# Optimization experiments

Measured on AMD Instinct MI355X. Metric: run time of the kernel, lower is better.

The kernel has to match this reference:

```python
import jax, jax.numpy as jnp
import numpy as np
from math import ceil

N, C_IN, HV, WV = 4, 3, 256, 256
C, K, NUM_LAYERS = 16, 3, 10
HK, WK = 45, 45
PROX_SCALE, KSCALE, KBSCALE, EPS = 10.0, 100.0, 0.01, 1e-8


def conv2_same(x, w):
    # torch F.conv2d (cross-correlation) with 'same' padding
    return jax.lax.conv_general_dilated(x, w, (1, 1), 'SAME',
                                        dimension_numbers=('NCHW', 'OIHW', 'NCHW'))


def pad_to(x, size):
    h, w = x.shape[-2], x.shape[-1]
    pads = [(0, 0)] * (x.ndim - 2) + [(0, size[0] - h), (0, size[1] - w)]
    return jnp.pad(x, pads)


def soft_threshold(x, b):
    return jnp.sign(x) * jax.nn.relu(jnp.abs(x) - b)


def circ_shift(x, s):
    return jnp.roll(x, (-s[0], -s[1]), axis=(-2, -1))


def csq(c):
    return (c * jnp.conj(c)).real


def forward(blurred_image, w0, ws, biases, kernel_biases, kernel_proxes, zetas, eta):
    Nb, C_in, Hv, Wv = blurred_image.shape
    Hs, Ws = Hv + HK - 1, Wv + WK - 1
    Hb, Wb = Hs + HK - 1, Ws + WK - 1
    fft_size = (int(ceil(Hb / 64.0) * 64), int(ceil(Wb / 64.0) * 64))
    rfft = lambda x: jnp.fft.rfft2(x, s=fft_size, axes=(-2, -1))
    irfft = lambda X: jnp.fft.irfft2(X, s=fft_size, axes=(-2, -1))

    # first-layer filter: zero-mean per (out,in) filter, then spatial reflect
    w_mean = w0.reshape(C, C_in, -1).mean(axis=-1)
    w0c = w0 - w_mean[:, :, None, None]
    w0_unreflected = jnp.transpose(w0c, (1, 0, 2, 3))   # (C_in, C, K, K)
    w0r = w0c[:, :, ::-1, ::-1]

    # analysis: cascade of convs, each feature stack padded to fft_size
    wy_list = []
    fy = blurred_image
    for layer in range(NUM_LAYERS):
        w = w0r if layer == 0 else ws[layer - 1]
        fy = conv2_same(fy, w)
        fy_p = pad_to(jnp.pad(fy, ((0, 0), (0, 0), (HK - 1, HK - 1), (WK - 1, WK - 1))), fft_size)
        wy_list.append(fy_p)

    delta = jnp.zeros((Nb, HK, WK), dtype=blurred_image.dtype).at[:, HK // 2, WK // 2].set(1.0)
    b0 = biases[0][None, :, None, None]
    z = soft_threshold(circ_shift(wy_list[-1], (HK // 2, WK // 2)), b0)
    Fz = rfft(z)
    k = delta
    Fg = None
    for layer in range(NUM_LAYERS):
        fy_p = wy_list.pop()
        Ffy = rfft(fy_p)                       # (N, C, H, Wf) complex
        Fk = rfft(k)[:, None]                  # (N, 1, H, Wf)
        zeta = PROX_SCALE * zetas[layer][None, :, None, None]
        num = zeta * (jnp.conj(Fk) * Ffy) + Fz
        den = zeta * csq(Fk) + 1.0
        Fg = num / (den + EPS)
        b = biases[layer + 1][None, :, None, None]
        z = soft_threshold(irfft(Fg), b)
        Fz = rfft(z)
        zk = kernel_proxes[layer]
        num_k = zk * jnp.sum(jnp.conj(Fz) * Ffy, axis=1) + Fk[:, 0]
        den_k = zk * jnp.sum(csq(Fz), axis=1) + 1.0
        k = irfft(num_k / (den_k + EPS))
        k_flat = k.reshape(Nb, -1)
        k_max = jax.scipy.special.logsumexp(k_flat * KSCALE, axis=-1) / KSCALE
        bk = KBSCALE * kernel_biases[layer]
        k = jax.nn.relu(k[:, :HK, :WK] - bk * k_max[:, None, None])
        k_sum = jnp.sum(k, axis=(1, 2), keepdims=True)
        k = (k + EPS * delta) / (k_sum + EPS)

    # final closed-form image solve in frequency domain (3-channel Cramer's rule)
    Fy = rfft(jnp.pad(blurred_image, ((0, 0), (0, 0), (HK - 1, HK - 1), (WK - 1, WK - 1))))
    Fk = rfft(k)                                # (N, H, Wf)
    Fw0 = rfft(circ_shift(pad_to(w0_unreflected, fft_size), (K // 2, K // 2)))  # (C_in, C, H, Wf)
    b_final = biases[NUM_LAYERS + 1][None, :, None, None]
    Fg = rfft(soft_threshold(irfft(Fg), b_final))

    eta_s = PROX_SCALE * eta[None, :, None, None]      # (1, C, 1, 1)
    Fwr, Fwg, Fwb = Fw0[0:1], Fw0[1:2], Fw0[2:3]       # (1, C, H, Wf)
    Fyr, Fyg, Fyb = Fy[:, 0], Fy[:, 1], Fy[:, 2]
    Fk_sq = csq(Fk)
    Crr = Fk_sq + jnp.sum(eta_s * csq(Fwr), axis=1)
    Cgg = Fk_sq + jnp.sum(eta_s * csq(Fwg), axis=1)
    Cbb = Fk_sq + jnp.sum(eta_s * csq(Fwb), axis=1)
    Crg = jnp.sum(eta_s * jnp.conj(Fwr) * Fwg, axis=1)
    Crb = jnp.sum(eta_s * jnp.conj(Fwr) * Fwb, axis=1)
    Cgb = jnp.sum(eta_s * jnp.conj(Fwg) * Fwb, axis=1)
    Fk_conj = jnp.conj(Fk)
    Br = Fk_conj * Fyr + jnp.sum(eta_s * jnp.conj(Fwr) * Fg, axis=1)
    Bg = Fk_conj * Fyg + jnp.sum(eta_s * jnp.conj(Fwg) * Fg, axis=1)
    Bb = Fk_conj * Fyb + jnp.sum(eta_s * jnp.conj(Fwb) * Fg, axis=1)
    Crg_sq, Crb_sq, Cgb_sq = csq(Crg), csq(Crb), csq(Cgb)
    Irr = Cgg * Cbb - Cgb_sq
    Igg = Crr * Cbb - Crb_sq
    Ibb = Crr * Cgg - Crg_sq
    Irg = jnp.conj(Cgb) * Crb - Cbb * Crg
    Irb = Crg * Cgb - Cgg * Crb
    Igb = jnp.conj(Crg) * Crb - Crr * Cgb
    den = (Crr * (Cgg * Cbb - Cgb_sq) - Cgg * Crb_sq - Cbb * Crg_sq
           + 2 * (Crg * Cgb * jnp.conj(Crb)).real) + EPS
    Fxr = Irr * Br + Irg * Bg + Irb * Bb
    Fxg = jnp.conj(Irg) * Br + Igg * Bg + Igb * Bb
    Fxb = jnp.conj(Irb) * Br + jnp.conj(Igb) * Bg + Ibb * Bb
    Fx = jnp.stack([Fxr, Fxg, Fxb], axis=1) / den[:, None]

    image = irfft(Fx)[:, :, HK // 2:HK // 2 + Hv, WK // 2:WK // 2 + Wv]
    return image, k


def setup_inputs() -> dict:
    key = jax.random.key(0)
    ks = jax.random.split(key, 4)

    def xavier(k, shape, fan_in, fan_out):
        std = (2.0 / (fan_in + fan_out)) ** 0.5
        return std * jax.random.normal(k, shape, dtype=jnp.float32)

    return {
        'blurred_image': jax.random.normal(ks[0], (N, C_IN, HV, WV), dtype=jnp.float32),
        'w0': xavier(ks[1], (C, C_IN, K, K), C_IN * K * K, C * K * K),
        'ws': xavier(ks[2], (NUM_LAYERS - 1, C, C, 3, 3), C * 9, C * 9),
        'biases': jnp.full((NUM_LAYERS + 2, C), 0.02, dtype=jnp.float32),
        'kernel_biases': jnp.zeros((NUM_LAYERS,), dtype=jnp.float32),
        'kernel_proxes': jnp.ones((NUM_LAYERS,), dtype=jnp.float32),
        'zetas': jnp.ones((NUM_LAYERS, C), dtype=jnp.float32),
        'eta': jnp.ones((C,), dtype=jnp.float32),
    }


def reference(blurred_image, w0, ws, biases, kernel_biases, kernel_proxes, zetas, eta):
    return forward(blurred_image, w0, ws, biases, kernel_biases, kernel_proxes, zetas, eta)
```

## Files before the change

kernel.cpp:

```cpp
#include <hip/hip_runtime.h>
#include <math.h>

#define FH 384
#define KF 193
#define KS 384
#define SPW 147456

typedef __attribute__((ext_vector_type(8))) short short8;
typedef __attribute__((ext_vector_type(4))) float f32x4;
typedef unsigned int u32;
typedef unsigned short u16;

static __device__ __forceinline__ float softt(float v, float b) {
    return copysignf(fmaxf(fabsf(v) - b, 0.f), v);
}
static __device__ __forceinline__ u16 bf16_rn(float v) {
    u32 u = __float_as_uint(v);
    u32 r = (u + 0x7FFFu + ((u >> 16) & 1u)) >> 16;
    return (u16)r;
}
static __device__ __forceinline__ float bf16_to_f(u16 h) {
    return __uint_as_float(((u32)h) << 16);
}
static __device__ __forceinline__ float2 ldc(const uint2* __restrict__ S, size_t i) {
    uint2 u = S[i];
    float2 r;
    r.x = __uint_as_float((u.x & 0xffffu) << 16) + __uint_as_float((u.y & 0xffffu) << 16);
    r.y = __uint_as_float(u.x & 0xffff0000u) + __uint_as_float(u.y & 0xffff0000u);
    return r;
}
static __device__ __forceinline__ uint2 packc(float re, float im) {
    u16 hr = bf16_rn(re), hi = bf16_rn(im);
    u16 lr = bf16_rn(re - bf16_to_f(hr)), li = bf16_rn(im - bf16_to_f(hi));
    uint2 o; o.x = (u32)hr | ((u32)hi << 16); o.y = (u32)lr | ((u32)li << 16);
    return o;
}

__global__ void init_ef_k(float2* Ef) {
    int idx = blockIdx.x * 256 + threadIdx.x;
    if (idx >= FH * FH) return;
    int h = idx / FH, j = idx % FH;
    int m = (h * j) % FH;
    float th = (float)(6.283185307179586 / FH) * (float)m;
    float2 v; v.x = cosf(th); v.y = -sinf(th);
    Ef[idx] = v;
}

__global__ void init_estack192(u16* __restrict__ H, u16* __restrict__ L, int inv)
{
    int idx = blockIdx.x * 256 + threadIdx.x;
    if (idx >= KS * KS) return;
    int gm = idx / KS, kp = idx % KS;
    int m = gm >> 1, comp = gm & 1;
    int t = kp >> 1, ri = kp & 1;
    int mm = (m * t) % 192;
    float th = (float)(6.283185307179586 / 192.0) * (float)mm;
    float c = cosf(th), s = sinf(th);
    float er, ei;
    if (inv) { er = c * (1.f/384.f); ei = s * (1.f/384.f); }
    else     { er = c;               ei = -s; }
    float v;
    if (comp == 0) v = (ri == 0) ? er : -ei;
    else           v = (ri == 0) ? ei :  er;
    u16 h = bf16_rn(v);
    H[idx] = h;
    L[idx] = bf16_rn(v - bf16_to_f(h));
}

// ... 54 lines not shown
    const u16*   iL  = inL0 ? inL0 + iofs : nullptr;
    u16* oH = outH0 + (size_t)blockIdx.z * 16*65536;
    u16* oL = outL0 + (size_t)blockIdx.z * 16*65536;
    __shared__ float tile[18][19];
    __shared__ float wl[16*16*9];
    int x0 = blockIdx.x * 16, y0 = blockIdx.y * 16;
    int t = threadIdx.x;
    int tx = t & 15, ty = t >> 4;
    int nw = 16 * Cin * 9;
    for (int i = t; i < nw; i += 256) {
        int d = i % 9;
        wl[i] = flip ? w[i + 8 - 2*d] : w[i];
    }
    float acc[16];
#pragma unroll
    for (int co = 0; co < 16; ++co) acc[co] = 0.f;
    for (int ci = 0; ci < Cin; ++ci) {
        __syncthreads();
        for (int i = t; i < 18*18; i += 256) {
            int yy = i / 18, xx = i % 18;
            int gy = y0 - 1 + yy, gx = x0 - 1 + xx;
            float v = 0.f;
            if (gy >= 0 && gy < 256 && gx >= 0 && gx < 256) {
                size_t ii = ((size_t)ci*256 + gy)*256 + gx;
                v = inF ? inF[ii] : (bf16_to_f(iH[ii]) + bf16_to_f(iL[ii]));
            }
            tile[yy][xx] = v;
        }
        __syncthreads();
        float v[9];
#pragma unroll
        for (int dy = 0; dy < 3; dy++)
#pragma unroll
            for (int dx = 0; dx < 3; dx++) v[dy*3+dx] = tile[ty+dy][tx+dx];
#pragma unroll
        for (int co = 0; co < 16; co++) {
            const float* wp = &wl[(co*Cin+ci)*9];
            acc[co] += v[0]*wp[0]+v[1]*wp[1]+v[2]*wp[2]
                     + v[3]*wp[3]+v[4]*wp[4]+v[5]*wp[5]
                     + v[6]*wp[6]+v[7]*wp[7]+v[8]*wp[8];
        }
    }
#pragma unroll
    for (int co = 0; co < 16; co++) {
        size_t o = ((size_t)co*256 + (y0+ty))*256 + (x0+tx);
        u16 h = bf16_rn(acc[co]);
        oH[o] = h;
        oL[o] = bf16_rn(acc[co] - bf16_to_f(h));
    }
}

__global__ void zinit_kernel(const u16* __restrict__ fy9H, const u16* __restrict__ fy9L,
                             const float* __restrict__ b0, float* __restrict__ z, int total)
{
    int idx = blockIdx.x*256 + threadIdx.x;
    if (idx >= total) return;
    int x = idx % FH; int r = idx / FH; int y = r % FH; int plane = r / FH;
    int c = plane & 15;
    int Y = y + 22; if (Y >= FH) Y -= FH;
    int X = x + 22; if (X >= FH) X -= FH;
    int yy = Y - 44, xx = X - 44;
    float v = 0.f;
    if (yy >= 0 && yy < 256 && xx >= 0 && xx < 256) {
        size_t ii = ((size_t)plane*256 + yy)*256 + xx;
        v = bf16_to_f(fy9H[ii]) + bf16_to_f(fy9L[ii]);
    }
    z[idx] = softt(v, b0[c]);
}

static __device__ __forceinline__ void r2c192_epilogue(
    f32x4 accA[2][4], f32x4 accB[2][4],
    int col0, int njN, int y0, int wave, int lm, int lq,
    uint2* __restrict__ outp, int B, int plane)
{
#pragma unroll
    for (int mi = 0; mi < 2; ++mi) {
#pragma unroll
        for (int nj = 0; nj < 4; ++nj) {
            if (nj >= njN) continue;
            int n = col0 + nj*16 + lm;
            int j = n >> 1;
            float pA[4], pB[4];
#pragma unroll
            for (int rr = 0; rr < 4; ++rr) {
                pA[rr] = __shfl_xor(accA[mi][nj][rr], 1);
                pB[rr] = __shfl_xor(accB[mi][nj][rr], 1);
            }
            if (((lm & 1) == 0) && j <= 96) {
                float th = (float)(6.283185307179586 / 384.0) * (float)j;
                float sv, cv;
                __sincosf(th, &sv, &cv);
                float wr = cv, wi = -sv;
                int ybase = y0 + wave*32 + mi*16 + lq*4;
#pragma unroll
                for (int rr = 0; rr < 4; ++rr) {
                    float ar = accA[mi][nj][rr], ai = pA[rr];
                    float br = accB[mi][nj][rr], bi = pB[rr];
                    float tr = wr*br - wi*bi;
                    float ti = wr*bi + wi*br;
                    size_t rowb = ((size_t)(ybase+rr)*B + plane)*KF;
                    outp[rowb + j] = packc(ar + tr, ai + ti);
                    if (j < 96) outp[rowb + 192 - j] = packc(ar - tr, -(ai - ti));
                }
            }
        }
    }
}

__global__ __launch_bounds__(256) void r2c192_f(
    const float* __restrict__ inp, int inH, int inW, int offY, int offX,
    const float* __restrict__ thr,
    const u16* __restrict__ TH, const u16* __restrict__ TL,
    uint2* __restrict__ outp, int B)
{
    __shared__ u16 AhS[2][8*64*8];
    __shared__ u16 AlS[2][8*64*8];
    int col0 = blockIdx.x * 64;
    int y0   = blockIdx.y * 128;
    int plane = blockIdx.z;
    int njN = (col0 >= 192) ? 1 : 4;
    int tid = threadIdx.x;
    int wave = tid >> 6, lane = tid & 63;
    int lm = lane & 15, lq = lane >> 4;
    f32x4 accA[2][4], accB[2][4];
#pragma unroll
    for (int mi = 0; mi < 2; ++mi)
#pragma unroll
        for (int nj = 0; nj < 4; ++nj) {
            accA[mi][nj] = (f32x4){0.f,0.f,0.f,0.f};
            accB[mi][nj] = (f32x4){0.f,0.f,0.f,0.f};
        }
    float bthr = thr ? thr[plane & 15] : 0.f;
    const float* inpP = inp + (size_t)plane*inH*inW;
    int mhi = (offX + inW) >> 1;
    for (int kt = 0; kt < mhi; kt += 32) {
#pragma unroll
        for (int s = 0; s < 4; ++s) {
            int slot = tid + s*256;
            int r = slot >> 3, kq = slot & 7;
            int yy = y0 + r - offY;
            int xx0 = 2*(kt + kq*4) - offX;
            float v[8];
#pragma unroll
            for (int d = 0; d < 8; ++d) {
                int xx = xx0 + d;
                float t = 0.f;
                if (yy >= 0 && yy < inH && xx >= 0 && xx < inW)
                    t = inpP[(size_t)yy*inW + xx];
                if (thr) t = softt(t, bthr);
                v[d] = t;
            }
            u16 h[8], l[8];
#pragma unroll
            for (int d = 0; d < 8; ++d) {
                h[d] = bf16_rn(v[d]);
                l[d] = bf16_rn(v[d] - bf16_to_f(h[d]));
            }
            int base = ((r >> 4)*64 + (r & 15) + 16*(kq >> 1))*8 + (kq & 1)*4;
            uint2 w;
            w.x = (u32)h[0] | ((u32)h[2] << 16); w.y = (u32)h[4] | ((u32)h[6] << 16);
            *(uint2*)&AhS[0][base] = w;
            w.x = (u32)h[1] | ((u32)h[3] << 16); w.y = (u32)h[5] | ((u32)h[7] << 16);
            *(uint2*)&AhS[1][base] = w;
            w.x = (u32)l[0] | ((u32)l[2] << 16); w.y = (u32)l[4] | ((u32)l[6] << 16);
            *(uint2*)&AlS[0][base] = w;
            w.x = (u32)l[1] | ((u32)l[3] << 16); w.y = (u32)l[5] | ((u32)l[7] << 16);
            *(uint2*)&AlS[1][base] = w;
        }
        __syncthreads();
        short8 A0h[2], A0l[2], A1h[2], A1l[2];
#pragma unroll
// ... 2 lines not shown
            A0h[mi] = *(const short8*)&AhS[0][fo];
            A0l[mi] = *(const short8*)&AlS[0][fo];
            A1h[mi] = *(const short8*)&AhS[1][fo];
            A1l[mi] = *(const short8*)&AlS[1][fo];
        }
#pragma unroll
        for (int nj = 0; nj < 4; ++nj) {
            if (nj >= njN) continue;
            size_t toff = (size_t)(col0 + nj*16 + lm)*192 + kt + lq*8;
            short8 Bh = *(const short8*)(TH + toff);
            short8 Bl = *(const short8*)(TL + toff);
#pragma unroll
            for (int mi = 0; mi < 2; ++mi) {
                accA[mi][nj] = __builtin_amdgcn_mfma_f32_16x16x32_bf16(A0h[mi], Bh, accA[mi][nj], 0, 0, 0);
                accA[mi][nj] = __builtin_amdgcn_mfma_f32_16x16x32_bf16(A0h[mi], Bl, accA[mi][nj], 0, 0, 0);
                accA[mi][nj] = __builtin_amdgcn_mfma_f32_16x16x32_bf16(A0l[mi], Bh, accA[mi][nj], 0, 0, 0);
                accB[mi][nj] = __builtin_amdgcn_mfma_f32_16x16x32_bf16(A1h[mi], Bh, accB[mi][nj], 0, 0, 0);
                accB[mi][nj] = __builtin_amdgcn_mfma_f32_16x16x32_bf16(A1h[mi], Bl, accB[mi][nj], 0, 0, 0);
                accB[mi][nj] = __builtin_amdgcn_mfma_f32_16x16x32_bf16(A1l[mi], Bh, accB[mi][nj], 0, 0, 0);
            }
        }
        __syncthreads();
    }
    r2c192_epilogue(accA, accB, col0, njN, y0, wave, lm, lq, outp, B, plane);
}

__global__ __launch_bounds__(256) void r2c192_s(
    const u16* __restrict__ Hs, const u16* __restrict__ Ls,
    int inH, int inW, int offY, int offX,
    const u16* __restrict__ TH, const u16* __restrict__ TL,
    uint2* __restrict__ outp, int B)
{
    __shared__ u16 AhS[2][8*64*8];
    __shared__ u16 AlS[2][8*64*8];
    int col0 = blockIdx.x * 64;
    int y0   = blockIdx.y * 128;
    int plane = blockIdx.z;
    int njN = (col0 >= 192) ? 1 : 4;
    int tid = threadIdx.x;
    int wave = tid >> 6, lane = tid & 63;
    int lm = lane & 15, lq = lane >> 4;
    f32x4 accA[2][4], accB[2][4];
#pragma unroll
    for (int mi = 0; mi < 2; ++mi)
#pragma unroll
        for (int nj = 0; nj < 4; ++nj) {
            accA[mi][nj] = (f32x4){0.f,0.f,0.f,0.f};
            accB[mi][nj] = (f32x4){0.f,0.f,0.f,0.f};
        }
    const u16* hP = Hs + (size_t)plane*inH*inW;
    const u16* lP = Ls + (size_t)plane*inH*inW;
    int mhi = (offX + inW) >> 1;
    for (int kt = 0; kt < mhi; kt += 32) {
#pragma unroll
        for (int s = 0; s < 4; ++s) {
            int slot = tid + s*256;
            int r = slot >> 3, kq = slot & 7;
            int yy = y0 + r - offY;
            int xx0 = 2*(kt + kq*4) - offX;
            uint2 hlo, hhi, llo, lhi;
            hlo.x=hlo.y=hhi.x=hhi.y=0u; llo.x=llo.y=lhi.x=lhi.y=0u;
            bool yok = (yy >= 0 && yy < inH);
            if (yok && xx0 >= 0 && xx0 + 4 <= inW) {
                size_t o = (size_t)yy*inW + xx0;
                hlo = *(const uint2*)(hP + o);
                llo = *(const uint2*)(lP + o);
            }
            if (yok && xx0 + 4 >= 0 && xx0 + 8 <= inW) {
                size_t o = (size_t)yy*inW + xx0 + 4;
                hhi = *(const uint2*)(hP + o);
                lhi = *(const uint2*)(lP + o);
            }
            int base = ((r >> 4)*64 + (r & 15) + 16*(kq >> 1))*8 + (kq & 1)*4;
            uint2 w;
            w.x = (hlo.x & 0xffffu) | (hlo.y << 16);
            w.y = (hhi.x & 0xffffu) | (hhi.y << 16);
            *(uint2*)&AhS[0][base] = w;
            w.x = (hlo.x >> 16) | (hlo.y & 0xffff0000u);
            w.y = (hhi.x >> 16) | (hhi.y & 0xffff0000u);
            *(uint2*)&AhS[1][base] = w;
            w.x = (llo.x & 0xffffu) | (llo.y << 16);
            w.y = (lhi.x & 0xffffu) | (lhi.y << 16);
            *(uint2*)&AlS[0][base] = w;
            w.x = (llo.x >> 16) | (llo.y & 0xffff0000u);
            w.y = (lhi.x >> 16) | (lhi.y & 0xffff0000u);
            *(uint2*)&AlS[1][base] = w;
        }
        __syncthreads();
        short8 A0h[2], A0l[2], A1h[2], A1l[2];
#pragma unroll
        for (int mi = 0; mi < 2; ++mi) {
            int fo = ((wave*2 + mi)*64 + lane)*8;
            A0h[mi] = *(const short8*)&AhS[0][fo];
            A0l[mi] = *(const short8*)&AlS[0][fo];
            A1h[mi] = *(const short8*)&AhS[1][fo];
            A1l[mi] = *(const short8*)&AlS[1][fo];
        }
#pragma unroll
        for (int nj = 0; nj < 4; ++nj) {
            if (nj >= njN) continue;
            size_t toff = (size_t)(col0 + nj*16 + lm)*192 + kt + lq*8;
            short8 Bh = *(const short8*)(TH + toff);
            short8 Bl = *(const short8*)(TL + toff);
#pragma unroll
            for (int mi = 0; mi < 2; ++mi) {
                accA[mi][nj] = __builtin_amdgcn_mfma_f32_16x16x32_bf16(A0h[mi], Bh, accA[mi][nj], 0, 0, 0);
                accA[mi][nj] = __builtin_amdgcn_mfma_f32_16x16x32_bf16(A0h[mi], Bl, accA[mi][nj], 0, 0, 0);
                accA[mi][nj] = __builtin_amdgcn_mfma_f32_16x16x32_bf16(A0l[mi], Bh, accA[mi][nj], 0, 0, 0);
                accB[mi][nj] = __builtin_amdgcn_mfma_f32_16x16x32_bf16(A1h[mi], Bh, accB[mi][nj], 0, 0, 0);
                accB[mi][nj] = __builtin_amdgcn_mfma_f32_16x16x32_bf16(A1h[mi], Bl, accB[mi][nj], 0, 0, 0);
                accB[mi][nj] = __builtin_amdgcn_mfma_f32_16x16x32_bf16(A1l[mi], Bh, accB[mi][nj], 0, 0, 0);
            }
        }
        __syncthreads();
    }
    r2c192_epilogue(accA, accB, col0, njN, y0, wave, lm, lq, outp, B, plane);
}

__global__ void gpm_kernel(uint2* __restrict__ S, int rows)
{
    int idx = blockIdx.x*256 + threadIdx.x;
    if (idx >= rows * 97) return;
    int j = idx % 97;
    size_t b = (size_t)(idx / 97) * KF;
    if (j == 96) {
        float2 f = ldc(S, b + 96);
        S[b + 96] = packc(2.f*f.x, -2.f*f.y);
    } else {
        float2 f1 = ldc(S, b + j);
        float2 f2 = ldc(S, b + 192 - j);
        float gpx = f1.x + f2.x, gpy = f1.y - f2.y;
        float hx  = f1.x - f2.x, hy  = f1.y + f2.y;
        float th = (float)(6.283185307179586 / 384.0) * (float)j;
        float sv, cv;
        __sincosf(th, &sv, &cv);
        float gmx = cv*hx - sv*hy;
        float gmy = cv*hy + sv*hx;
        S[b + j]       = packc(gpx, gpy);
        S[b + 192 - j] = packc(gmx, gmy);
    }
}

__global__ __launch_bounds__(256) void c2r192(
    const uint2* __restrict__ Ain,
    const u16* __restrict__ UH, const u16* __restrict__ UL,
    float* __restrict__ outp, const float* __restrict__ thr,
    u16* __restrict__ spH, u16* __restrict__ spL, int B)
{
    __shared__ u16 AhS[2][8*64*8];
    __shared__ u16 AlS[2][8*64*8];
    int col0 = blockIdx.x * 64;
    int y0   = blockIdx.y * 128;
    int plane = blockIdx.z;
    int tid = threadIdx.x;
    int wave = tid >> 6, lane = tid & 63;
    int lm = lane & 15, lq = lane >> 4;
    f32x4 accP[2][4], accQ[2][4];
#pragma unroll
    for (int mi = 0; mi < 2; ++mi)
#pragma unroll
// ... 58 lines not shown
                accQ[mi][nj] = __builtin_amdgcn_mfma_f32_16x16x32_bf16(A1h[mi], Bl, accQ[mi][nj], 0, 0, 0);
                accQ[mi][nj] = __builtin_amdgcn_mfma_f32_16x16x32_bf16(A1l[mi], Bh, accQ[mi][nj], 0, 0, 0);
            }
        }
        __syncthreads();
    }
    float bthr = thr ? thr[plane & 15] : 0.f;
#pragma unroll
    for (int mi = 0; mi < 2; ++mi) {
#pragma unroll
        for (int nj = 0; nj < 4; ++nj) {
            int m = col0 + nj*16 + lm;
#pragma unroll
            for (int rr = 0; rr < 4; ++rr) {
                int y = y0 + wave*32 + mi*16 + lq*4 + rr;
                float xe = accP[mi][nj][rr];
                float xo = accQ[mi][nj][rr];
                float2 o2; o2.x = xe; o2.y = xo;
                *(float2*)&outp[((size_t)plane*FH + y)*FH + 2*m] = o2;
                if (spH) {
                    float s0 = softt(xe, bthr), s1 = softt(xo, bthr);
                    u16 h0 = bf16_rn(s0), h1 = bf16_rn(s1);
                    u16 l0 = bf16_rn(s0 - bf16_to_f(h0)), l1 = bf16_rn(s1 - bf16_to_f(h1));
                    size_t d = (size_t)plane*SPW + (size_t)y*FH + 2*m;
                    *(u32*)&spH[d] = (u32)h0 | ((u32)h1 << 16);
                    *(u32*)&spL[d] = (u32)l0 | ((u32)l1 << 16);
                }
            }
        }
    }
}

__global__ __launch_bounds__(256) void zgemm_col_mfma2(
    const u16* __restrict__ EH, const u16* __restrict__ EL,
    const uint2* __restrict__ Bm, uint2* __restrict__ Cm, int N, float sgn)
{
    __shared__ u16 BhS[2][4*64*8];
    __shared__ u16 BlS[2][4*64*8];
    int col0 = blockIdx.x * 64;
    int row0 = blockIdx.y * 128;
    int tid = threadIdx.x;
    int wave = tid >> 6, lane = tid & 63;
    int lm = lane & 15, lq = lane >> 4;
    f32x4 accE[2][4], accO[2][4];
#pragma unroll
    for (int mi = 0; mi < 2; ++mi)
#pragma unroll
        for (int nj = 0; nj < 4; ++nj) {
            accE[mi][nj] = (f32x4){0.f,0.f,0.f,0.f};
            accO[mi][nj] = (f32x4){0.f,0.f,0.f,0.f};
        }
    int arow0 = row0 + wave*32 + lm;
    for (int kt = 0; kt < KS; kt += 32) {
        int tbase = kt >> 1;
#pragma unroll
        for (int s = 0; s < 4; ++s) {
            int slot = tid + s*256;
            int p    = slot >> 9;
            int inr  = slot & 511;
            int pair = inr >> 6;
            int n    = inr & 63;
            int gn   = col0 + n;
            int t0   = tbase + pair*2;
            uint2 u0, u1;
            u0.x = u0.y = u1.x = u1.y = 0u;
            if (gn < N) {
                u0 = Bm[(size_t)(2*t0 + p)*N + gn];
                u1 = Bm[(size_t)(2*t0 + 2 + p)*N + gn];
            }
            int ntile = n >> 4, n0 = n & 15;
            int lrow  = (pair >> 1)*16 + n0;
            int base  = (ntile*64 + lrow)*8 + (pair & 1)*4;
            uint2 hp, lp;
            hp.x = u0.x; hp.y = u1.x;
            lp.x = u0.y; lp.y = u1.y;
            *(uint2*)&BhS[p][base] = hp;
// ... 18 lines not shown
                accE[mi][nj] = __builtin_amdgcn_mfma_f32_16x16x32_bf16(Ah[mi], Bh0, accE[mi][nj], 0, 0, 0);
                accE[mi][nj] = __builtin_amdgcn_mfma_f32_16x16x32_bf16(Ah[mi], Bl0, accE[mi][nj], 0, 0, 0);
                accE[mi][nj] = __builtin_amdgcn_mfma_f32_16x16x32_bf16(Al[mi], Bh0, accE[mi][nj], 0, 0, 0);
                accO[mi][nj] = __builtin_amdgcn_mfma_f32_16x16x32_bf16(Ah[mi], Bh1, accO[mi][nj], 0, 0, 0);
                accO[mi][nj] = __builtin_amdgcn_mfma_f32_16x16x32_bf16(Ah[mi], Bl1, accO[mi][nj], 0, 0, 0);
                accO[mi][nj] = __builtin_amdgcn_mfma_f32_16x16x32_bf16(Al[mi], Bh1, accO[mi][nj], 0, 0, 0);
            }
        }
        __syncthreads();
    }
#pragma unroll
    for (int mi = 0; mi < 2; ++mi) {
#pragma unroll
        for (int nj = 0; nj < 4; ++nj) {
            int coln = col0 + nj*16 + lm;
            if (coln < N) {
                int r0 = row0 + wave*32 + mi*16 + lq*4;
                int h  = r0 >> 1;
#pragma unroll
                for (int pp = 0; pp < 2; ++pp) {
                    float e_re = accE[mi][nj][2*pp],   e_im = accE[mi][nj][2*pp+1];
                    float o_re = accO[mi][nj][2*pp],   o_im = accO[mi][nj][2*pp+1];
                    int hh = h + pp;
                    float th = (float)(6.283185307179586 / 384.0) * (float)hh;
                    float sv, cv;
                    __sincosf(th, &sv, &cv);
                    float twr = cv, twi = sgn * sv;
                    float tr = twr*o_re - twi*o_im;
                    float ti = twr*o_im + twi*o_re;
                    Cm[(size_t)hh*N + coln]         = packc(e_re + tr, e_im + ti);
                    Cm[(size_t)(hh + 192)*N + coln] = packc(e_re - tr, e_im - ti);
                }
            }
        }
    }
}

__global__ void fg_kernel(const uint2* __restrict__ Ffy, uint2* __restrict__ Fz,
                          const uint2* __restrict__ Fk, const float* __restrict__ zetas,
                          int L, int total)
{
    int idx = blockIdx.x*256 + threadIdx.x;
    if (idx >= total) return;
    int k = idx % KF; int r = idx / KF;
    int c = r & 15; int hi = r >> 4;
    float zeta = 10.f * zetas[L*16 + c];
    float2 fk = ldc(Fk, (size_t)hi*KF + k);
    float2 fy = ldc(Ffy, idx);
    float2 fz = ldc(Fz, idx);
    float nx = zeta*(fk.x*fy.x + fk.y*fy.y) + fz.x;
// ... 37 lines not shown
{
    int img = blockIdx.y;
    const float* kraw = kraw0 + (size_t)img*FH*FH;
    int b = blockIdx.x, t = threadIdx.x;
    float m = -1e30f, s = 0.f;
    for (int i = b*256 + t; i < FH*FH; i += 64*256) {
        float v = 100.f * kraw[i];
        lse_comb(m, s, v, 1.f);
    }
    __shared__ float sm[256], ss[256];
    sm[t] = m; ss[t] = s;
    __syncthreads();
    for (int st = 128; st > 0; st >>= 1) {
        if (t < st) {
            float mm = sm[t], sc = ss[t];
            lse_comb(mm, sc, sm[t+st], ss[t+st]);
            sm[t] = mm; ss[t] = sc;
        }
        __syncthreads();
    }
    if (t == 0) { float2 o; o.x = sm[0]; o.y = ss[0]; parts[img*64 + b] = o; }
}

__global__ void lse_final_kernel(const float2* __restrict__ parts, float* __restrict__ kmaxB)
{
    int img = blockIdx.x;
    int t = threadIdx.x;
    __shared__ float sm[64], ss[64];
    float2 p = parts[img*64 + t];
    sm[t] = p.x; ss[t] = p.y;
    __syncthreads();
    for (int st = 32; st > 0; st >>= 1) {
        if (t < st) {
            float mm = sm[t], sc = ss[t];
            lse_comb(mm, sc, sm[t+st], ss[t+st]);
            sm[t] = mm; ss[t] = sc;
        }
        __syncthreads();
    }
    if (t == 0) kmaxB[img] = (sm[0] + logf(ss[0])) * 0.01f;
}

__global__ void zero_kernel(float* __restrict__ p, int n)
{
    int i = blockIdx.x*256 + threadIdx.x;
    if (i < n) p[i] = 0.f;
}

__global__ void kdelta_kernel(float* __restrict__ kful, int G)
{
    int t = threadIdx.x;
    if (t < G) kful[(size_t)t*FH*FH + 22*FH + 22] = 1.f;
}

__global__ __launch_bounds__(256) void knew_kernel(const float* __restrict__ kraw0,
    const float* __restrict__ kmax, const float* __restrict__ kb, int L,
    float* __restrict__ kful0)
{
    int img = blockIdx.x;
    const float* kraw = kraw0 + (size_t)img*FH*FH;
    float*       kful = kful0 + (size_t)img*FH*FH;
    int t = threadIdx.x;
    float thr = 0.01f * kb[L] * kmax[img];
    float vs[8]; float loc = 0.f;
#pragma unroll
    for (int ii = 0; ii < 8; ++ii) {
        int i = t + ii*256;
        float v = 0.f;
        if (i < 45*45) {
            int y = i/45, x = i - y*45;
            v = fmaxf(kraw[y*FH + x] - thr, 0.f);
        }
        vs[ii] = v; loc += v;
    }
    __shared__ float sr[256];
    sr[t] = loc; __syncthreads();
    for (int st = 128; st > 0; st >>= 1) { if (t < st) sr[t] += sr[t+st]; __syncthreads(); }
    float den = sr[0] + 1e-8f;
#pragma unroll
    for (int ii = 0; ii < 8; ++ii) {
        int i = t + ii*256;
        if (i < 45*45) {
            int y = i/45, x = i - y*45;
            float v = vs[ii] + ((y == 22 && x == 22) ? 1e-8f : 0.f);
            kful[y*FH + x] = v / den;
        }
// ... 108 lines not shown
    int x = rem % 45; int y = rem / 45;
    outp[idx] = kful[(size_t)img*FH*FH + y*FH + x];
}

extern "C" void kernel_launch(void* const* d_in, const int* in_sizes, int n_in,
                              void* d_out, int out_size, void* d_ws, size_t ws_size,
                              hipStream_t stream)
{
    (void)in_sizes; (void)n_in; (void)out_size;
    const float* blurred = (const float*)d_in[0];
    const float* w0      = (const float*)d_in[1];
    const float* wsw     = (const float*)d_in[2];
    const float* biases  = (const float*)d_in[3];
    const float* kbias   = (const float*)d_in[4];
    const float* kprox   = (const float*)d_in[5];
    const float* zetas   = (const float*)d_in[6];
    const float* eta     = (const float*)d_in[7];
    float* outp = (float*)d_out;

    auto al = [](size_t b) { return (b + 255) & ~(size_t)255; };
    auto need = [&](int G) -> size_t {
        size_t s = 0;
        s += al((size_t)FH*FH*8);
        s += 4*al((size_t)KS*KS*2);
        s += 2*al((size_t)208*192*2);
        s += 2*al((size_t)192*224*2);
        s += al(432*4);
        s += 2*al((size_t)10*G*16*65536*2);
        s += al((size_t)G*16*FH*FH*4);
        s += 2*al((size_t)G*16*SPW*2);
        s += 3*al((size_t)G*16*FH*KF*8);
        s += 3*al((size_t)G*FH*KF*8);
        s += 2*al((size_t)G*FH*FH*4);
        s += 2*al((size_t)G*3*FH*KF*8);
        s += al((size_t)G*64*8) + al(256);
        return s;
    };
    int G = 4;
    while (G > 1 && need(G) > ws_size) G >>= 1;

    char* base = (char*)d_ws;
    size_t off = 0;
    auto alloc = [&](size_t bytes) -> void* {
        void* p = (void*)(base + off);
        off += (bytes + 255) & ~(size_t)255;
        return p;
    };
    float2* Ef   = (float2*)alloc((size_t)FH*FH*8);
    u16* EfH = (u16*)alloc((size_t)KS*KS*2);
    u16* EfL = (u16*)alloc((size_t)KS*KS*2);
    u16* EiH = (u16*)alloc((size_t)KS*KS*2);
    u16* EiL = (u16*)alloc((size_t)KS*KS*2);
    u16* T1H = (u16*)alloc((size_t)208*192*2);
    u16* T1L = (u16*)alloc((size_t)208*192*2);
    u16* U1H = (u16*)alloc((size_t)192*224*2);
    u16* U1L = (u16*)alloc((size_t)192*224*2);
    float*  w0cB = (float*)alloc(432*4);
    u16*    fyH  = (u16*)alloc((size_t)10*G*16*65536*2);
    u16*    fyL  = (u16*)alloc((size_t)10*G*16*65536*2);
    float*  zsp  = (float*)alloc((size_t)G*16*FH*FH*4);
    u16*    zspSH= (u16*)alloc((size_t)G*16*SPW*2);
    u16*    zspSL= (u16*)alloc((size_t)G*16*SPW*2);
    uint2*  mid  = (uint2*)alloc((size_t)G*16*FH*KF*8);
    uint2*  FzFg = (uint2*)alloc((size_t)G*16*FH*KF*8);
    uint2*  Ffy  = (uint2*)alloc((size_t)G*16*FH*KF*8);
    uint2*  Fk   = (uint2*)alloc((size_t)G*FH*KF*8);
    uint2*  kfA  = (uint2*)alloc((size_t)G*FH*KF*8);
    uint2*  kfB  = (uint2*)alloc((size_t)G*FH*KF*8);
    float*  kraw = (float*)alloc((size_t)G*FH*FH*4);
    float*  kful = (float*)alloc((size_t)G*FH*FH*4);
    uint2*  FyB  = (uint2*)alloc((size_t)G*3*FH*KF*8);
    uint2*  FxB  = (uint2*)alloc((size_t)G*3*FH*KF*8);
    float2* lseP = (float2*)alloc((size_t)G*64*8);
    float*  kmaxB= (float*)alloc(256);
    float2* Fw0B = (float2*)fyH;

    init_ef_k<<<(FH*FH+255)/256, 256, 0, stream>>>(Ef);
    init_estack192<<<(KS*KS+255)/256, 256, 0, stream>>>(EfH, EfL, 0);
    init_estack192<<<(KS*KS+255)/256, 256, 0, stream>>>(EiH, EiL, 1);
    init_t192<<<(208*192+255)/256, 256, 0, stream>>>(T1H, T1L);
    init_u192<<<(192*224+255)/256, 256, 0, stream>>>(U1H, U1L);
    w0c_kernel<<<1, 64, 0, stream>>>(w0, w0cB);

    auto zgf = [&](const uint2* Bm, uint2* Cm, int Ncols) {
        zgemm_col_mfma2<<<dim3((Ncols+63)/64, 3), 256, 0, stream>>>(
            EfH, EfL, Bm, Cm, Ncols, -1.f);
    };
    auto zgi = [&](const uint2* Bm, uint2* Cm, int Ncols) {
        zgemm_col_mfma2<<<dim3((Ncols+63)/64, 3), 256, 0, stream>>>(
            EiH, EiL, Bm, Cm, Ncols, 1.f);
    };
    auto r2c = [&](const float* inp, int inH, int inW, int oY, int oX,
                   const float* thr, uint2* o, int B) {
        r2c192_f<<<dim3(4, 3, B), 256, 0, stream>>>(
            inp, inH, inW, oY, oX, thr, T1H, T1L, o, B);
    };
    auto r2cs = [&](const u16* Hs, const u16* Ls, int inH, int inW, int oY, int oX,
                    uint2* o, int B) {
        r2c192_s<<<dim3(4, 3, B), 256, 0, stream>>>(
            Hs, Ls, inH, inW, oY, oX, T1H, T1L, o, B);
    };
    auto c2r = [&](uint2* Ain, float* o, int B,
                   const float* thr, u16* sH, u16* sL) {
        int rows = FH * B;
        gpm_kernel<<<(rows*97 + 255)/256, 256, 0, stream>>>(Ain, rows);
        c2r192<<<dim3(3, 3, B), 256, 0, stream>>>(
            Ain, U1H, U1L, o, thr, sH, sL, B);
    };

    const size_t CKL = (size_t)G*16*65536;

    for (int g0 = 0; g0 < 4; g0 += G) {
        const float* img = blurred + (size_t)g0*3*65536;

        conv3x3_kernel<<<dim3(16,16,G), 256, 0, stream>>>(
            img, nullptr, nullptr, w0cB, fyH, fyL, 3, 1, (size_t)3*65536);
        for (int l = 1; l < 10; ++l)
            conv3x3_kernel<<<dim3(16,16,G), 256, 0, stream>>>(
                nullptr, fyH + (size_t)(l-1)*CKL, fyL + (size_t)(l-1)*CKL,
                wsw + (size_t)(l-1)*2304,
                fyH + (size_t)l*CKL, fyL + (size_t)l*CKL, 16, 0, (size_t)16*65536);

        int totZ = G*16*FH*FH;
        zinit_kernel<<<(totZ+255)/256, 256, 0, stream>>>(
            fyH + 9*CKL, fyL + 9*CKL, biases, zsp, totZ);
        r2c(zsp, FH, FH, 0, 0, nullptr, mid, G*16);
        zgf(mid, FzFg, G*16*KF);

        zero_kernel<<<(G*FH*FH+255)/256, 256, 0, stream>>>(kful, G*FH*FH);
        kdelta_kernel<<<1, 64, 0, stream>>>(kful, G);

        int totS = G*16*FH*KF;
        int totK = G*FH*KF;
        for (int it = 0; it < 10; ++it) {
            int Lfy = 9 - it;
            r2cs(fyH + (size_t)Lfy*CKL, fyL + (size_t)Lfy*CKL, 256, 256, 44, 44, mid, G*16);
            zgf(mid, Ffy, G*16*KF);
            r2c(kful, FH, FH, 0, 0, nullptr, mid, G);
            zgf(mid, Fk, G*KF);
            fg_kernel<<<(totS+255)/256, 256, 0, stream>>>(Ffy, FzFg, Fk, zetas, it, totS);
            zgi(FzFg, mid, G*16*KF);
            c2r(mid, zsp, G*16, biases + (it+1)*16, zspSH, zspSL);
            r2cs(zspSH, zspSL, FH, FH, 0, 0, mid, G*16);
            zgf(mid, FzFg, G*16*KF);
            knum_kernel<<<(totK+255)/256, 256, 0, stream>>>(FzFg, Ffy, Fk, kprox, it, totK, kfA);
            zgi(kfA, kfB, G*KF);
            c2r(kfB, kraw, G, nullptr, nullptr, nullptr);
            lse_part_kernel<<<dim3(64,G), 256, 0, stream>>>(kraw, lseP);
            lse_final_kernel<<<G, 64, 0, stream>>>(lseP, kmaxB);
            knew_kernel<<<G, 256, 0, stream>>>(kraw, kmaxB, kbias, it, kful);
        }

        r2c(img, 256, 256, 44, 44, nullptr, mid, 3*G);
        zgf(mid, FyB, 3*G*KF);
        r2c(kful, FH, FH, 0, 0, nullptr, mid, G);
        zgf(mid, Fk, G*KF);
        r2c(zsp, FH, FH, 0, 0, biases + 11*16, mid, G*16);
        zgf(mid, FzFg, G*16*KF);
        fw0_kernel<<<(48*FH*KF+255)/256, 256, 0, stream>>>(w0cB, Ef, Fw0B);
        wiener_kernel<<<(totK+255)/256, 256, 0, stream>>>(Fk, FyB, Fw0B, FzFg, eta, G, totK, FxB);
        zgi(FxB, mid, 3*G*KF);
        c2r(mid, zsp, 3*G, nullptr, nullptr, nullptr);
        int totC = G*3*65536;
        crop_kernel<<<(totC+255)/256, 256, 0, stream>>>(zsp, outp + (size_t)g0*3*65536, totC);
        int totKC = G*2025;
        kcopy_kernel<<<(totKC+255)/256, 256, 0, stream>>>(kful, outp + 786432 + g0*2025, totKC);
    }
}
```

Measured before the change: 8.760 ms.

## De-interleave bf16 split storage, prune kernel FFT, table twiddles, fuse LSE final

Conv outputs, the z init buffer and the c2r sparse outputs are now stored with even and odd columns in separate half-rows. This lets r2c192_s load 8 contiguous bf16 values with 16-byte vector loads instead of gathering and repacking in registers. The kernel-estimate FFT only transforms the 45x45 support: one row block, and the column GEMM's K loop is cut to 64. Twiddle sincos calls are replaced by a precomputed table, and lse_final is folded into knew_kernel to save one launch per iteration. The risks are layout mismatches between producers and consumers, and scalar u16 stores in c2r in place of packed u32 stores.

```diff
diff --git a/kernel.cpp b/kernel.cpp
--- a/kernel.cpp
+++ b/kernel.cpp
@@ -44,6 +44,15 @@
     float th = (float)(6.283185307179586 / FH) * (float)m;
     float2 v; v.x = cosf(th); v.y = -sinf(th);
     Ef[idx] = v;
+}
+
+__global__ void init_tw(float2* twT) {
+    int i = blockIdx.x * 256 + threadIdx.x;
+    if (i < 193) {
+        float th = (float)(6.283185307179586 / 384.0) * (float)i;
+        float2 v; v.x = cosf(th); v.y = sinf(th);
+        twT[i] = v;
+    }
 }
 
 __global__ void init_estack192(u16* __restrict__ H, u16* __restrict__ L, int inv)
@@ -144,7 +153,9 @@
             int gy = y0 - 1 + yy, gx = x0 - 1 + xx;
             float v = 0.f;
             if (gy >= 0 && gy < 256 && gx >= 0 && gx < 256) {
-                size_t ii = ((size_t)ci*256 + gy)*256 + gx;
+                size_t ii;
+                if (inF) ii = ((size_t)ci*256 + gy)*256 + gx;
+                else     ii = ((size_t)ci*256 + gy)*256 + ((gx>>1) + (gx&1)*128);
                 v = inF ? inF[ii] : (bf16_to_f(iH[ii]) + bf16_to_f(iL[ii]));
             }
             tile[yy][xx] = v;
@@ -163,9 +174,11 @@
                      + v[6]*wp[6]+v[7]*wp[7]+v[8]*wp[8];
         }
     }
+    int xo = x0 + tx;
+    int xd = (xo >> 1) + (xo & 1)*128;
 #pragma unroll
     for (int co = 0; co < 16; co++) {
-        size_t o = ((size_t)co*256 + (y0+ty))*256 + (x0+tx);
+        size_t o = ((size_t)co*256 + (y0+ty))*256 + xd;
         u16 h = bf16_rn(acc[co]);
         oH[o] = h;
         oL[o] = bf16_rn(acc[co] - bf16_to_f(h));
@@ -173,7 +186,8 @@
 }
 
 __global__ void zinit_kernel(const u16* __restrict__ fy9H, const u16* __restrict__ fy9L,
-                             const float* __restrict__ b0, float* __restrict__ z, int total)
+                             const float* __restrict__ b0,
+                             u16* __restrict__ oH, u16* __restrict__ oL, int total)
 {
     int idx = blockIdx.x*256 + threadIdx.x;
     if (idx >= total) return;
@@ -184,15 +198,20 @@
     int yy = Y - 44, xx = X - 44;
     float v = 0.f;
     if (yy >= 0 && yy < 256 && xx >= 0 && xx < 256) {
-        size_t ii = ((size_t)plane*256 + yy)*256 + xx;
+        size_t ii = ((size_t)plane*256 + yy)*256 + ((xx>>1) + (xx&1)*128);
         v = bf16_to_f(fy9H[ii]) + bf16_to_f(fy9L[ii]);
     }
-    z[idx] = softt(v, b0[c]);
+    float s = softt(v, b0[c]);
+    u16 h = bf16_rn(s);
+    size_t d = (size_t)plane*SPW + (size_t)y*FH + ((x>>1) + (x&1)*192);
+    oH[d] = h;
+    oL[d] = bf16_rn(s - bf16_to_f(h));
 }
 
 static __device__ __forceinline__ void r2c192_epilogue(
     f32x4 accA[2][4], f32x4 accB[2][4],
     int col0, int njN, int y0, int wave, int lm, int lq,
+    const float2* __restrict__ twT,
     uint2* __restrict__ outp, int B, int plane)
 {
 #pragma unroll
@@ -209,10 +228,8 @@
                 pB[rr] = __shfl_xor(accB[mi][nj][rr], 1);
             }
             if (((lm & 1) == 0) && j <= 96) {
-                float th = (float)(6.283185307179586 / 384.0) * (float)j;
-                float sv, cv;
-                __sincosf(th, &sv, &cv);
-                float wr = cv, wi = -sv;
+                float2 tw = twT[j];
+                float wr = tw.x, wi = -tw.y;
                 int ybase = y0 + wave*32 + mi*16 + lq*4;
 #pragma unroll
                 for (int rr = 0; rr < 4; ++rr) {
@@ -230,9 +247,11 @@
 }
 
 __global__ __launch_bounds__(256) void r2c192_f(
-    const float* __restrict__ inp, int inH, int inW, int offY, int offX,
+    const float* __restrict__ inp, int inH, int inW, int inStride, size_t planeStride,
+    int offY, int offX,
     const float* __restrict__ thr,
     const u16* __restrict__ TH, const u16* __restrict__ TL,
+    const float2* __restrict__ twT,
     uint2* __restrict__ outp, int B)
 {
     __shared__ u16 AhS[2][8*64*8];
@@ -253,7 +272,7 @@
             accB[mi][nj] = (f32x4){0.f,0.f,0.f,0.f};
         }
     float bthr = thr ? thr[plane & 15] : 0.f;
-    const float* inpP = inp + (size_t)plane*inH*inW;
+    const float* inpP = inp + (size_t)plane*planeStride;
     int mhi = (offX + inW) >> 1;
     for (int kt = 0; kt < mhi; kt += 32) {
 #pragma unroll
@@ -268,7 +287,7 @@
                 int xx = xx0 + d;
                 float t = 0.f;
                 if (yy >= 0 && yy < inH && xx >= 0 && xx < inW)
-                    t = inpP[(size_t)yy*inW + xx];
+                    t = inpP[(size_t)yy*inStride + xx];
                 if (thr) t = softt(t, bthr);
                 v[d] = t;
             }
@@ -317,13 +336,14 @@
         }
         __syncthreads();
     }
-    r2c192_epilogue(accA, accB, col0, njN, y0, wave, lm, lq, outp, B, plane);
+    r2c192_epilogue(accA, accB, col0, njN, y0, wave, lm, lq, twT, outp, B, plane);
 }
 
 __global__ __launch_bounds__(256) void r2c192_s(
     const u16* __restrict__ Hs, const u16* __restrict__ Ls,
     int inH, int inW, int offY, int offX,
     const u16* __restrict__ TH, const u16* __restrict__ TL,
+    const float2* __restrict__ twT,
     uint2* __restrict__ outp, int B)
 {
     __shared__ u16 AhS[2][8*64*8];
@@ -345,41 +365,48 @@
         }
     const u16* hP = Hs + (size_t)plane*inH*inW;
     const u16* lP = Ls + (size_t)plane*inH*inW;
+    int W2  = inW >> 1;
+    int ox2 = offX >> 1;
+    bool al16 = ((ox2 & 7) == 0);
     int mhi = (offX + inW) >> 1;
     for (int kt = 0; kt < mhi; kt += 32) {
 #pragma unroll
         for (int s = 0; s < 4; ++s) {
             int slot = tid + s*256;
-            int r = slot >> 3, kq = slot & 7;
+            int p    = slot >> 9;
+            int inr  = slot & 511;
+            int r = inr >> 2, kq2 = inr & 3;
             int yy = y0 + r - offY;
-            int xx0 = 2*(kt + kq*4) - offX;
-            uint2 hlo, hhi, llo, lhi;
-            hlo.x=hlo.y=hhi.x=hhi.y=0u; llo.x=llo.y=lhi.x=lhi.y=0u;
-            bool yok = (yy >= 0 && yy < inH);
-            if (yok && xx0 >= 0 && xx0 + 4 <= inW) {
-                size_t o = (size_t)yy*inW + xx0;
-                hlo = *(const uint2*)(hP + o);
-                llo = *(const uint2*)(lP + o);
-            }
-            if (yok && xx0 + 4 >= 0 && xx0 + 8 <= inW) {
-                size_t o = (size_t)yy*inW + xx0 + 4;
-                hhi = *(const uint2*)(hP + o);
-                lhi = *(const uint2*)(lP + o);
-            }
-            int base = ((r >> 4)*64 + (r & 15) + 16*(kq >> 1))*8 + (kq & 1)*4;
-            uint2 w;
-            w.x = (hlo.x & 0xffffu) | (hlo.y << 16);
-            w.y = (hhi.x & 0xffffu) | (hhi.y << 16);
-            *(uint2*)&AhS[0][base] = w;
-            w.x = (hlo.x >> 16) | (hlo.y & 0xffff0000u);
-            w.y = (hhi.x >> 16) | (hhi.y & 0xffff0000u);
-            *(uint2*)&AhS[1][base] = w;
-            w.x = (llo.x & 0xffffu) | (llo.y << 16);
-            w.y = (lhi.x & 0xffffu) | (lhi.y << 16);
-            *(uint2*)&AlS[0][base] = w;
-            w.x = (llo.x >> 16) | (llo.y & 0xffff0000u);
-            w.y = (lhi.x >> 16) | (lhi.y & 0xffff0000u);
-            *(uint2*)&AlS[1][base] = w;
+            int m0 = kt + kq2*8;
+            int pos = m0 - ox2;
+            uint4 hq = {0u,0u,0u,0u}, lq4 = {0u,0u,0u,0u};
+            if (yy >= 0 && yy < inH) {
+                const u16* hr = hP + (size_t)yy*inW + (size_t)p*W2;
+                const u16* lr = lP + (size_t)yy*inW + (size_t)p*W2;
+                if (pos >= 0 && pos + 8 <= W2) {
+                    if (al16) {
+                        hq  = *(const uint4*)(hr + pos);
+                        lq4 = *(const uint4*)(lr + pos);
+                    } else {
+                        hq.x = *(const u32*)(hr+pos);   hq.y = *(const u32*)(hr+pos+2);
+                        hq.z = *(const u32*)(hr+pos+4); hq.w = *(const u32*)(hr+pos+6);
+                        lq4.x = *(const u32*)(lr+pos);   lq4.y = *(const u32*)(lr+pos+2);
+                        lq4.z = *(const u32*)(lr+pos+4); lq4.w = *(const u32*)(lr+pos+6);
+                    }
+                } else if (pos + 8 > 0 && pos < W2) {
+#pragma unroll
+                    for (int q = 0; q < 4; ++q) {
+                        int pp = pos + 2*q;
+                        if (pp >= 0 && pp + 2 <= W2) {
+                            ((u32*)&hq)[q]  = *(const u32*)(hr+pp);
+                            ((u32*)&lq4)[q] = *(const u32*)(lr+pp);
+                        }
+                    }
+                }
+            }
+            int base = ((r >> 4)*64 + (r & 15) + 16*kq2)*8;
+            *(uint4*)&AhS[p][base] = hq;
+            *(uint4*)&AlS[p][base] = lq4;
         }
         __syncthreads();
         short8 A0h[2], A0l[2], A1h[2], A1l[2];
@@ -409,10 +436,10 @@
         }
         __syncthreads();
     }
-    r2c192_epilogue(accA, accB, col0, njN, y0, wave, lm, lq, outp, B, plane);
-}
-
-__global__ void gpm_kernel(uint2* __restrict__ S, int rows)
+    r2c192_epilogue(accA, accB, col0, njN, y0, wave, lm, lq, twT, outp, B, plane);
+}
+
+__global__ void gpm_kernel(uint2* __restrict__ S, const float2* __restrict__ twT, int rows)
 {
     int idx = blockIdx.x*256 + threadIdx.x;
     if (idx >= rows * 97) return;
@@ -426,11 +453,9 @@
         float2 f2 = ldc(S, b + 192 - j);
         float gpx = f1.x + f2.x, gpy = f1.y - f2.y;
         float hx  = f1.x - f2.x, hy  = f1.y + f2.y;
-        float th = (float)(6.283185307179586 / 384.0) * (float)j;
-        float sv, cv;
-        __sincosf(th, &sv, &cv);
-        float gmx = cv*hx - sv*hy;
-        float gmy = cv*hy + sv*hx;
+        float2 tw = twT[j];
+        float gmx = tw.x*hx - tw.y*hy;
+        float gmy = tw.x*hy + tw.y*hx;
         S[b + j]       = packc(gpx, gpy);
         S[b + 192 - j] = packc(gmx, gmy);
     }
@@ -535,9 +560,9 @@
                     float s0 = softt(xe, bthr), s1 = softt(xo, bthr);
                     u16 h0 = bf16_rn(s0), h1 = bf16_rn(s1);
                     u16 l0 = bf16_rn(s0 - bf16_to_f(h0)), l1 = bf16_rn(s1 - bf16_to_f(h1));
-                    size_t d = (size_t)plane*SPW + (size_t)y*FH + 2*m;
-                    *(u32*)&spH[d] = (u32)h0 | ((u32)h1 << 16);
-                    *(u32*)&spL[d] = (u32)l0 | ((u32)l1 << 16);
+                    size_t d = (size_t)plane*SPW + (size_t)y*FH + m;
+                    spH[d]       = h0; spL[d]       = l0;
+                    spH[d + 192] = h1; spL[d + 192] = l1;
                 }
             }
         }
@@ -546,7 +571,8 @@
 
 __global__ __launch_bounds__(256) void zgemm_col_mfma2(
     const u16* __restrict__ EH, const u16* __restrict__ EL,
-    const uint2* __restrict__ Bm, uint2* __restrict__ Cm, int N, float sgn)
+    const uint2* __restrict__ Bm, uint2* __restrict__ Cm, int N, float sgn,
+    int ktHi, const float2* __restrict__ twT)
 {
     __shared__ u16 BhS[2][4*64*8];
     __shared__ u16 BlS[2][4*64*8];
@@ -564,7 +590,7 @@
             accO[mi][nj] = (f32x4){0.f,0.f,0.f,0.f};
         }
     int arow0 = row0 + wave*32 + lm;
-    for (int kt = 0; kt < KS; kt += 32) {
+    for (int kt = 0; kt < ktHi; kt += 32) {
         int tbase = kt >> 1;
 #pragma unroll
         for (int s = 0; s < 4; ++s) {
@@ -629,10 +655,8 @@
                     float e_re = accE[mi][nj][2*pp],   e_im = accE[mi][nj][2*pp+1];
                     float o_re = accO[mi][nj][2*pp],   o_im = accO[mi][nj][2*pp+1];
                     int hh = h + pp;
-                    float th = (float)(6.283185307179586 / 384.0) * (float)hh;
-                    float sv, cv;
-                    __sincosf(th, &sv, &cv);
-                    float twr = cv, twi = sgn * sv;
+                    float2 tw = twT[hh];
+                    float twr = tw.x, twi = sgn * tw.y;
                     float tr = twr*o_re - twi*o_im;
                     float ti = twr*o_im + twi*o_re;
                     Cm[(size_t)hh*N + coln]         = packc(e_re + tr, e_im + ti);
@@ -716,13 +740,28 @@
     if (t == 0) { float2 o; o.x = sm[0]; o.y = ss[0]; parts[img*64 + b] = o; }
 }
 
-__global__ void lse_final_kernel(const float2* __restrict__ parts, float* __restrict__ kmaxB)
+__global__ void zero_kernel(float* __restrict__ p, int n)
+{
+    int i = blockIdx.x*256 + threadIdx.x;
+    if (i < n) p[i] = 0.f;
+}
+
+__global__ void kdelta_kernel(float* __restrict__ kful, int G)
+{
+    int t = threadIdx.x;
+    if (t < G) kful[(size_t)t*FH*FH + 22*FH + 22] = 1.f;
+}
+
+__global__ __launch_bounds__(256) void knew_kernel(const float2* __restrict__ parts,
+    const float* __restrict__ kraw0, const float* __restrict__ kb, int L,
+    float* __restrict__ kful0)
 {
     int img = blockIdx.x;
+    const float* kraw = kraw0 + (size_t)img*FH*FH;
+    float*       kful = kful0 + (size_t)img*FH*FH;
     int t = threadIdx.x;
     __shared__ float sm[64], ss[64];
-    float2 p = parts[img*64 + t];
-    sm[t] = p.x; ss[t] = p.y;
+    if (t < 64) { float2 p = parts[img*64 + t]; sm[t] = p.x; ss[t] = p.y; }
     __syncthreads();
     for (int st = 32; st > 0; st >>= 1) {
         if (t < st) {
@@ -732,30 +771,8 @@
         }
         __syncthreads();
     }
-    if (t == 0) kmaxB[img] = (sm[0] + logf(ss[0])) * 0.01f;
-}
-
-__global__ void zero_kernel(float* __restrict__ p, int n)
-{
-    int i = blockIdx.x*256 + threadIdx.x;
-    if (i < n) p[i] = 0.f;
-}
-
-__global__ void kdelta_kernel(float* __restrict__ kful, int G)
-{
-    int t = threadIdx.x;
-    if (t < G) kful[(size_t)t*FH*FH + 22*FH + 22] = 1.f;
-}
-
-__global__ __launch_bounds__(256) void knew_kernel(const float* __restrict__ kraw0,
-    const float* __restrict__ kmax, const float* __restrict__ kb, int L,
-    float* __restrict__ kful0)
-{
-    int img = blockIdx.x;
-    const float* kraw = kraw0 + (size_t)img*FH*FH;
-    float*       kful = kful0 + (size_t)img*FH*FH;
-    int t = threadIdx.x;
-    float thr = 0.01f * kb[L] * kmax[img];
+    float kmax = (sm[0] + logf(ss[0])) * 0.01f;
+    float thr = 0.01f * kb[L] * kmax;
     float vs[8]; float loc = 0.f;
 #pragma unroll
     for (int ii = 0; ii < 8; ++ii) {
@@ -910,6 +927,7 @@
     auto need = [&](int G) -> size_t {
         size_t s = 0;
         s += al((size_t)FH*FH*8);
+        s += al(193*8);
         s += 4*al((size_t)KS*KS*2);
         s += 2*al((size_t)208*192*2);
         s += 2*al((size_t)192*224*2);
@@ -921,7 +939,7 @@
         s += 3*al((size_t)G*FH*KF*8);
         s += 2*al((size_t)G*FH*FH*4);
         s += 2*al((size_t)G*3*FH*KF*8);
-        s += al((size_t)G*64*8) + al(256);
+        s += al((size_t)G*64*8);
         return s;
     };
     int G = 4;
@@ -935,6 +953,7 @@
         return p;
     };
     float2* Ef   = (float2*)alloc((size_t)FH*FH*8);
+    float2* twT  = (float2*)alloc(193*8);
     u16* EfH = (u16*)alloc((size_t)KS*KS*2);
     u16* EfL = (u16*)alloc((size_t)KS*KS*2);
     u16* EiH = (u16*)alloc((size_t)KS*KS*2);
@@ -960,10 +979,10 @@
     uint2*  FyB  = (uint2*)alloc((size_t)G*3*FH*KF*8);
     uint2*  FxB  = (uint2*)alloc((size_t)G*3*FH*KF*8);
     float2* lseP = (float2*)alloc((size_t)G*64*8);
-    float*  kmaxB= (float*)alloc(256);
     float2* Fw0B = (float2*)fyH;
 
     init_ef_k<<<(FH*FH+255)/256, 256, 0, stream>>>(Ef);
+    init_tw<<<1, 256, 0, stream>>>(twT);
     init_estack192<<<(KS*KS+255)/256, 256, 0, stream>>>(EfH, EfL, 0);
     init_estack192<<<(KS*KS+255)/256, 256, 0, stream>>>(EiH, EiL, 1);
     init_t192<<<(208*192+255)/256, 256, 0, stream>>>(T1H, T1L);
@@ -972,28 +991,34 @@
 
     auto zgf = [&](const uint2* Bm, uint2* Cm, int Ncols) {
         zgemm_col_mfma2<<<dim3((Ncols+63)/64, 3), 256, 0, stream>>>(
-            EfH, EfL, Bm, Cm, Ncols, -1.f);
+            EfH, EfL, Bm, Cm, Ncols, -1.f, KS, twT);
     };
     auto zgi = [&](const uint2* Bm, uint2* Cm, int Ncols) {
         zgemm_col_mfma2<<<dim3((Ncols+63)/64, 3), 256, 0, stream>>>(
-            EiH, EiL, Bm, Cm, Ncols, 1.f);
+            EiH, EiL, Bm, Cm, Ncols, 1.f, KS, twT);
     };
     auto r2c = [&](const float* inp, int inH, int inW, int oY, int oX,
                    const float* thr, uint2* o, int B) {
         r2c192_f<<<dim3(4, 3, B), 256, 0, stream>>>(
-            inp, inH, inW, oY, oX, thr, T1H, T1L, o, B);
+            inp, inH, inW, inW, (size_t)inH*inW, oY, oX, thr, T1H, T1L, twT, o, B);
     };
     auto r2cs = [&](const u16* Hs, const u16* Ls, int inH, int inW, int oY, int oX,
                     uint2* o, int B) {
         r2c192_s<<<dim3(4, 3, B), 256, 0, stream>>>(
-            Hs, Ls, inH, inW, oY, oX, T1H, T1L, o, B);
+            Hs, Ls, inH, inW, oY, oX, T1H, T1L, twT, o, B);
     };
     auto c2r = [&](uint2* Ain, float* o, int B,
                    const float* thr, u16* sH, u16* sL) {
         int rows = FH * B;
-        gpm_kernel<<<(rows*97 + 255)/256, 256, 0, stream>>>(Ain, rows);
+        gpm_kernel<<<(rows*97 + 255)/256, 256, 0, stream>>>(Ain, twT, rows);
         c2r192<<<dim3(3, 3, B), 256, 0, stream>>>(
             Ain, U1H, U1L, o, thr, sH, sL, B);
+    };
+    auto r2ck = [&]() {
+        r2c192_f<<<dim3(4, 1, G), 256, 0, stream>>>(
+            kful, 45, 45, FH, (size_t)FH*FH, 0, 0, nullptr, T1H, T1L, twT, mid, G);
+        zgemm_col_mfma2<<<dim3((G*KF+63)/64, 3), 256, 0, stream>>>(
+            EfH, EfL, mid, Fk, G*KF, -1.f, 64, twT);
     };
 
     const size_t CKL = (size_t)G*16*65536;
@@ -1011,8 +1036,8 @@
 
         int totZ = G*16*FH*FH;
         zinit_kernel<<<(totZ+255)/256, 256, 0, stream>>>(
-            fyH + 9*CKL, fyL + 9*CKL, biases, zsp, totZ);
-        r2c(zsp, FH, FH, 0, 0, nullptr, mid, G*16);
+            fyH + 9*CKL, fyL + 9*CKL, biases, zspSH, zspSL, totZ);
+        r2cs(zspSH, zspSL, FH, FH, 0, 0, mid, G*16);
         zgf(mid, FzFg, G*16*KF);
 
         zero_kernel<<<(G*FH*FH+255)/256, 256, 0, stream>>>(kful, G*FH*FH);
@@ -1024,8 +1049,7 @@
             int Lfy = 9 - it;
             r2cs(fyH + (size_t)Lfy*CKL, fyL + (size_t)Lfy*CKL, 256, 256, 44, 44, mid, G*16);
             zgf(mid, Ffy, G*16*KF);
-            r2c(kful, FH, FH, 0, 0, nullptr, mid, G);
-            zgf(mid, Fk, G*KF);
+            r2ck();
             fg_kernel<<<(totS+255)/256, 256, 0, stream>>>(Ffy, FzFg, Fk, zetas, it, totS);
             zgi(FzFg, mid, G*16*KF);
             c2r(mid, zsp, G*16, biases + (it+1)*16, zspSH, zspSL);
@@ -1035,14 +1059,12 @@
             zgi(kfA, kfB, G*KF);
             c2r(kfB, kraw, G, nullptr, nullptr, nullptr);
             lse_part_kernel<<<dim3(64,G), 256, 0, stream>>>(kraw, lseP);
-            lse_final_kernel<<<G, 64, 0, stream>>>(lseP, kmaxB);
-            knew_kernel<<<G, 256, 0, stream>>>(kraw, kmaxB, kbias, it, kful);
+            knew_kernel<<<G, 256, 0, stream>>>(lseP, kraw, kbias, it, kful);
         }
 
         r2c(img, 256, 256, 44, 44, nullptr, mid, 3*G);
         zgf(mid, FyB, 3*G*KF);
-        r2c(kful, FH, FH, 0, 0, nullptr, mid, G);
-        zgf(mid, Fk, G*KF);
+        r2ck();
         r2c(zsp, FH, FH, 0, 0, biases + 11*16, mid, G*16);
         zgf(mid, FzFg, G*16*KF);
         fw0_kernel<<<(48*FH*KF+255)/256, 256, 0, stream>>>(w0cB, Ef, Fw0B);
```

New measurement: 8.726 ms. No clear change (-0.4%).
